# Kernel tuning notes

Hardware: AMD Instinct MI355X
Metric: run time of the kernel (lower is better)

Reference implementation:

```python
import jax, jax.numpy as jnp
import numpy as np

N_SLOTS = 24   # n_slots from __init__
N_ITERS = 25   # fixed Lloyd iterations (stand-in for sklearn max_iter/convergence)
NORM_EPS = 1e-12  # torch F.normalize eps


def setup_inputs() -> dict:
    key = jax.random.key(0)
    features = jax.random.normal(key, (32, 4096, 256), dtype=jnp.float32)
    return {"features": features}


def _pairwise_sqdist(x, x_sq, centers):
    # x: [B,N,D], x_sq: [B,N,1], centers: [B,K,D] -> [B,N,K]
    c_sq = jnp.sum(centers * centers, axis=-1)  # [B,K]
    return x_sq - 2.0 * jnp.einsum('bnd,bkd->bnk', x, centers) + c_sq[:, None, :]


def _kmeans_batched(x, k, n_iters):
    # x: [B,N,D] -> centers [B,K,D], assignments [B,N]
    B, N, D = x.shape
    # deterministic init: K evenly-spaced points per batch item
    init_idx = jnp.linspace(0, N - 1, k).astype(jnp.int32)
    centers0 = x[:, init_idx, :]  # [B,K,D]
    x_sq = jnp.sum(x * x, axis=-1, keepdims=True)  # [B,N,1]

    def step(centers, _):
        d = _pairwise_sqdist(x, x_sq, centers)          # [B,N,K]
        assign = jnp.argmin(d, axis=-1)                 # [B,N]
        onehot = jax.nn.one_hot(assign, k, dtype=x.dtype)  # [B,N,K]
        counts = jnp.sum(onehot, axis=1)                # [B,K]
        sums = jnp.einsum('bnk,bnd->bkd', onehot, x)    # [B,K,D] scatter-mean numerator
        new_centers = sums / jnp.maximum(counts, 1.0)[..., None]
        # empty clusters keep their previous center
        new_centers = jnp.where(counts[..., None] > 0, new_centers, centers)
        return new_centers, None

    centers, _ = jax.lax.scan(step, centers0, None, length=n_iters)
    final_assign = jnp.argmin(_pairwise_sqdist(x, x_sq, centers), axis=-1)
    return centers, final_assign


def reference(features):
    # L2-normalize along feature dim (use_l2_normalization=True)
    norm = jnp.sqrt(jnp.sum(features * features, axis=-1, keepdims=True))
    f = features / jnp.maximum(norm, NORM_EPS)
    # original detaches before clustering (sklearn on CPU): no gradient flow
    f = jax.lax.stop_gradient(f)
    centers, assign = _kmeans_batched(f, N_SLOTS, N_ITERS)
    # slot masks: one_hot then transpose(-2,-1) -> [B, K, N] float32
    slot_masks = jax.nn.one_hot(assign, N_SLOTS, dtype=jnp.float32).transpose(0, 2, 1)
    return centers, slot_masks
```

## Files before the change

### kernel.cpp

```cpp
#include <hip/hip_runtime.h>
#include <math.h>


#define BATCH 32
#define NPTS 4096
#define DIM 256
#define NSLOT 24
#define NITER 25

__global__ __launch_bounds__(256) void k_norm(const float* __restrict__ feat,
                                              double* __restrict__ inv_norm) {
  int lane = threadIdx.x & 63;
  int wid = threadIdx.x >> 6;
  int p = blockIdx.x * 4 + wid;
  const float4 v = *(const float4*)(feat + (size_t)p * DIM + lane * 4);
  double s = (double)v.x * v.x + (double)v.y * v.y + (double)v.z * v.z + (double)v.w * v.w;
#pragma unroll
  for (int m = 32; m; m >>= 1) s += __shfl_xor(s, m);
  if (lane == 0) inv_norm[p] = 1.0 / fmax(sqrt(s), 1e-12);
}

__device__ __forceinline__ double block_sum_256(double v, double* red) {
#pragma unroll
  for (int m = 32; m; m >>= 1) v += __shfl_xor(v, m);
  int w = threadIdx.x >> 6;
  if ((threadIdx.x & 63) == 0) red[w] = v;
  __syncthreads();
  return red[0] + red[1] + red[2] + red[3];
}

__global__ __launch_bounds__(256) void k_init_centers(const float* __restrict__ feat,
                                                      const double* __restrict__ inv_norm,
                                                      double* __restrict__ centers,
                                                      float* __restrict__ cT32,
                                                      float* __restrict__ c_sq32) {
  __shared__ double red[4];
  int t = threadIdx.x, k = blockIdx.x, b = blockIdx.y;
  int idx = (int)((double)k * (NPTS - 1) / (NSLOT - 1));
  double v = (double)feat[((size_t)b * NPTS + idx) * DIM + t] * inv_norm[b * NPTS + idx];
  centers[((size_t)b * NSLOT + k) * DIM + t] = v;
  cT32[((size_t)b * DIM + t) * NSLOT + k] = (float)v;
  double s = block_sum_256(v * v, red);
  if (t == 0) c_sq32[b * NSLOT + k] = (float)s;
}

__global__ __launch_bounds__(256) void k_transpose(const float* __restrict__ feat,
                                                   float* __restrict__ xT) {
  __shared__ float tile[64][65];
  int ix = threadIdx.x & 63, iy = threadIdx.x >> 6;
  int bx = blockIdx.x, by = blockIdx.y, b = blockIdx.z;
  const float* fb = feat + ((size_t)b * NPTS + bx * 64) * DIM + by * 64;
#pragma unroll
  for (int r = 0; r < 64; r += 4)
    tile[r + iy][ix] = fb[(size_t)(r + iy) * DIM + ix];
  __syncthreads();
  float* xb = xT + ((size_t)b * DIM + by * 64) * NPTS + bx * 64;
#pragma unroll
  for (int r = 0; r < 64; r += 4)
    xb[(size_t)(r + iy) * NPTS + ix] = tile[ix][r + iy];
}

template <bool USE_T>
__global__ __launch_bounds__(256) void k_assign(const float* __restrict__ feat,
                                                const float* __restrict__ xT,
                                                const double* __restrict__ inv_norm,
                                                const float* __restrict__ cT32,
                                                const float* __restrict__ c_sq32,
                                                int* __restrict__ assign) {
  __shared__ float part[3][64][NSLOT + 1];
  int lane = threadIdx.x & 63;
  int q = __builtin_amdgcn_readfirstlane(threadIdx.x >> 6);
  int blk = blockIdx.x, b = blockIdx.y;
  int n = blk * 64 + lane;
  const float* cb = cT32 + ((size_t)b * DIM + q * 64) * NSLOT;

  float dot[NSLOT];
#pragma unroll
  for (int k = 0; k < NSLOT; ++k) dot[k] = 0.0f;

  for (int d = 0; d < 64; d += 4) {
    float x0, x1, x2, x3;
    if (USE_T) {
      const float* xp = xT + ((size_t)b * DIM + q * 64 + d) * NPTS + n;
      x0 = xp[0]; x1 = xp[NPTS]; x2 = xp[2 * NPTS]; x3 = xp[3 * NPTS];
    } else {
      float4 v = *(const float4*)(feat + ((size_t)b * NPTS + n) * DIM + q * 64 + d);
      x0 = v.x; x1 = v.y; x2 = v.z; x3 = v.w;
    }
    const float* cp = cb + (size_t)d * NSLOT;
#pragma unroll
    for (int k = 0; k < NSLOT; ++k) {
      float s = dot[k];
      s = fmaf(x0, cp[k], s);
      s = fmaf(x1, cp[NSLOT + k], s);
      s = fmaf(x2, cp[2 * NSLOT + k], s);
      s = fmaf(x3, cp[3 * NSLOT + k], s);
      dot[k] = s;
    }
  }

  if (q) {
#pragma unroll
    for (int k = 0; k < NSLOT; ++k) part[q - 1][lane][k] = dot[k];
  }
  __syncthreads();

  if (q == 0) {
    float inv = (float)inv_norm[b * NPTS + n];
    const float* csq = c_sq32 + b * NSLOT;
    int a = 0;
    float best = 0.0f;
#pragma unroll
    for (int k = 0; k < NSLOT; ++k) {
      float df = dot[k] + part[0][lane][k] + part[1][lane][k] + part[2][lane][k];
      float s = csq[k] - 2.0f * (df * inv);
      if (k == 0) { best = s; }
      else if (s < best) { best = s; a = k; }
    }
    assign[b * NPTS + n] = a;
  }
}

__global__ __launch_bounds__(256) void k_cluster(const float* __restrict__ feat,
                                                 const double* __restrict__ inv_norm,
                                                 const int* __restrict__ assign,
                                                 double* __restrict__ centers,
                                                 float* __restrict__ cT32,
                                                 float* __restrict__ c_sq32) {
  __shared__ int list[NPTS];
  __shared__ int wtot[4];
  __shared__ double part[4][DIM];
  __shared__ double red[4];

  int id = blockIdx.x;
  int xcd = id & 7;
  int r = id >> 3;
  int k = r % NSLOT;
  int b = (r / NSLOT) * 8 + xcd;

  int t = threadIdx.x;
  int lane = t & 63;
  int w = __builtin_amdgcn_readfirstlane(t >> 6);

  const int* ab = assign + b * NPTS;
  int base = 0;
  for (int rr = 0; rr < NPTS / 256; ++rr) {
    int a = ab[rr * 256 + t];
    bool m = (a == k);
    unsigned long long bal = __ballot(m);
    int rank = __popcll(bal & ((1ull << lane) - 1ull));
    if (lane == 0) wtot[w] = __popcll(bal);
    __syncthreads();
    int off = base;
#pragma unroll
    for (int w2 = 0; w2 < 3; ++w2)
      if (w2 < w) off += wtot[w2];
    if (m) list[off + rank] = rr * 256 + t;
    base += wtot[0] + wtot[1] + wtot[2] + wtot[3];
    __syncthreads();
  }
  int mcount = base;

  const float* fb = feat + (size_t)b * NPTS * DIM + lane * 4;
  const double* ib = inv_norm + b * NPTS;
  double a0 = 0.0, a1 = 0.0, a2 = 0.0, a3 = 0.0;

  for (int i = w; i < mcount; i += 8) {
    int n0 = __builtin_amdgcn_readfirstlane(list[i]);
    bool have1 = (i + 4) < mcount;
    int n1 = __builtin_amdgcn_readfirstlane(have1 ? list[i + 4] : list[i]);
    float4 v0 = *(const float4*)(fb + (size_t)n0 * DIM);
    float4 v1 = *(const float4*)(fb + (size_t)n1 * DIM);
    double i0 = ib[n0];
    double i1 = ib[n1];
    a0 += (double)v0.x * i0; a1 += (double)v0.y * i0;
    a2 += (double)v0.z * i0; a3 += (double)v0.w * i0;
    if (have1) {
      a0 += (double)v1.x * i1; a1 += (double)v1.y * i1;
      a2 += (double)v1.z * i1; a3 += (double)v1.w * i1;
    }
  }

  part[w][lane * 4 + 0] = a0;
  part[w][lane * 4 + 1] = a1;
  part[w][lane * 4 + 2] = a2;
  part[w][lane * 4 + 3] = a3;
  __syncthreads();

  double s = ((part[0][t] + part[1][t]) + part[2][t]) + part[3][t];

  size_t ci = ((size_t)b * NSLOT + k) * DIM + t;
  double nc = (mcount > 0) ? (s / (double)mcount) : centers[ci];
  centers[ci] = nc;
  cT32[((size_t)b * DIM + t) * NSLOT + k] = (float)nc;
  double sq = block_sum_256(nc * nc, red);
  if (t == 0) c_sq32[b * NSLOT + k] = (float)sq;
}

__global__ __launch_bounds__(256) void k_mask(const int* __restrict__ assign,
                                              float* __restrict__ masks) {
  int t = threadIdx.x, nc = blockIdx.x, k = blockIdx.y, b = blockIdx.z;
  int n = nc * 256 + t;
  masks[((size_t)b * NSLOT + k) * NPTS + n] = (assign[b * NPTS + n] == k) ? 1.0f : 0.0f;
}

__global__ __launch_bounds__(256) void k_copyc(const double* __restrict__ centers,
                                               float* __restrict__ out_centers) {
  int t = threadIdx.x, k = blockIdx.x, b = blockIdx.y;
  size_t i = ((size_t)b * NSLOT + k) * DIM + t;
  out_centers[i] = (float)centers[i];
}

extern "C" void kernel_launch(void* const* d_in, const int* in_sizes, int n_in,
                              void* d_out, int out_size, void* d_ws, size_t ws_size,
                              hipStream_t stream) {
  (void)in_sizes; (void)n_in; (void)out_size;
  const float* feat = (const float*)d_in[0];
  float* out_centers = (float*)d_out;
  float* out_masks = out_centers + (size_t)BATCH * NSLOT * DIM;

  char* ws = (char*)d_ws;
  double* inv_norm = (double*)ws; ws += (size_t)BATCH * NPTS * 8;
  double* centers  = (double*)ws; ws += (size_t)BATCH * NSLOT * DIM * 8;
  float* cT32      = (float*)ws;  ws += (size_t)BATCH * DIM * NSLOT * 4;
  float* c_sq32    = (float*)ws;  ws += (size_t)BATCH * NSLOT * 4;
  int* assign      = (int*)ws;    ws += (size_t)BATCH * NPTS * 4;
  float* xT        = (float*)ws;
  size_t need_xT = (size_t)(ws - (char*)d_ws) + (size_t)BATCH * DIM * NPTS * 4;
  bool useT = ws_size >= need_xT;

  k_norm<<<BATCH * NPTS / 4, 256, 0, stream>>>(feat, inv_norm);
  k_init_centers<<<dim3(NSLOT, BATCH), 256, 0, stream>>>(feat, inv_norm, centers,
                                                         cT32, c_sq32);
  if (useT)
    k_transpose<<<dim3(NPTS / 64, DIM / 64, BATCH), 256, 0, stream>>>(feat, xT);

  for (int it = 0; it <= NITER; ++it) {
    if (useT)
      k_assign<true><<<dim3(NPTS / 64, BATCH), 256, 0, stream>>>(feat, xT, inv_norm,
                                                                 cT32, c_sq32, assign);
    else
      k_assign<false><<<dim3(NPTS / 64, BATCH), 256, 0, stream>>>(feat, xT, inv_norm,
                                                                  cT32, c_sq32, assign);
    if (it == NITER) break;
    k_cluster<<<NSLOT * BATCH, 256, 0, stream>>>(feat, inv_norm, assign,
                                                 centers, cT32, c_sq32);
  }

  k_mask<<<dim3(NPTS / 256, NSLOT, BATCH), 256, 0, stream>>>(assign, out_masks);
  k_copyc<<<dim3(NSLOT, BATCH), 256, 0, stream>>>(centers, out_centers);
}
```

Baseline: 1.862 ms.

## Split cluster accumulation into point quarters with separate reduction kernel

The per-cluster center update is split so each (batch, slot) is handled by four blocks, each scanning a quarter of the points, writing partial sums and counts to global memory. A new small kernel combines the four partials and computes the new centers, the transposed fp32 copy and the squared norms. The gather loop is unrolled to four rows per step and the assign kernel's inner loop now loads 8 dims per iteration. This raises the block count for the gather phase and its memory-level parallelism, at the cost of an extra launch per iteration and a partial-sum buffer round trip. The XCD-aware batch mapping is dropped.

```diff
diff --git a/kernel.cpp b/kernel.cpp
--- a/kernel.cpp
+++ b/kernel.cpp
@@ -7,6 +7,7 @@
 #define DIM 256
 #define NSLOT 24
 #define NITER 25
+#define QPTS 1024
 
 __global__ __launch_bounds__(256) void k_norm(const float* __restrict__ feat,
                                               double* __restrict__ inv_norm) {
@@ -78,23 +79,24 @@
 #pragma unroll
   for (int k = 0; k < NSLOT; ++k) dot[k] = 0.0f;
 
-  for (int d = 0; d < 64; d += 4) {
-    float x0, x1, x2, x3;
+  for (int d = 0; d < 64; d += 8) {
+    float x[8];
     if (USE_T) {
       const float* xp = xT + ((size_t)b * DIM + q * 64 + d) * NPTS + n;
-      x0 = xp[0]; x1 = xp[NPTS]; x2 = xp[2 * NPTS]; x3 = xp[3 * NPTS];
+#pragma unroll
+      for (int j = 0; j < 8; ++j) x[j] = xp[(size_t)j * NPTS];
     } else {
       float4 v = *(const float4*)(feat + ((size_t)b * NPTS + n) * DIM + q * 64 + d);
-      x0 = v.x; x1 = v.y; x2 = v.z; x3 = v.w;
+      float4 u = *(const float4*)(feat + ((size_t)b * NPTS + n) * DIM + q * 64 + d + 4);
+      x[0] = v.x; x[1] = v.y; x[2] = v.z; x[3] = v.w;
+      x[4] = u.x; x[5] = u.y; x[6] = u.z; x[7] = u.w;
     }
     const float* cp = cb + (size_t)d * NSLOT;
 #pragma unroll
     for (int k = 0; k < NSLOT; ++k) {
       float s = dot[k];
-      s = fmaf(x0, cp[k], s);
-      s = fmaf(x1, cp[NSLOT + k], s);
-      s = fmaf(x2, cp[2 * NSLOT + k], s);
-      s = fmaf(x3, cp[3 * NSLOT + k], s);
+#pragma unroll
+      for (int j = 0; j < 8; ++j) s = fmaf(x[j], cp[j * NSLOT + k], s);
       dot[k] = s;
     }
   }
@@ -121,32 +123,29 @@
   }
 }
 
-__global__ __launch_bounds__(256) void k_cluster(const float* __restrict__ feat,
-                                                 const double* __restrict__ inv_norm,
-                                                 const int* __restrict__ assign,
-                                                 double* __restrict__ centers,
-                                                 float* __restrict__ cT32,
-                                                 float* __restrict__ c_sq32) {
-  __shared__ int list[NPTS];
+__global__ __launch_bounds__(256) void k_cluster4(const float* __restrict__ feat,
+                                                  const double* __restrict__ inv_norm,
+                                                  const int* __restrict__ assign,
+                                                  double* __restrict__ psumG,
+                                                  int* __restrict__ cntG) {
+  __shared__ unsigned short list[QPTS];
   __shared__ int wtot[4];
   __shared__ double part[4][DIM];
-  __shared__ double red[4];
 
   int id = blockIdx.x;
-  int xcd = id & 7;
-  int r = id >> 3;
+  int q = id & 3;
+  int r = id >> 2;
   int k = r % NSLOT;
-  int b = (r / NSLOT) * 8 + xcd;
+  int b = r / NSLOT;
 
   int t = threadIdx.x;
   int lane = t & 63;
   int w = __builtin_amdgcn_readfirstlane(t >> 6);
 
-  const int* ab = assign + b * NPTS;
+  const int* ab = assign + b * NPTS + q * QPTS;
   int base = 0;
-  for (int rr = 0; rr < NPTS / 256; ++rr) {
-    int a = ab[rr * 256 + t];
-    bool m = (a == k);
+  for (int rr = 0; rr < QPTS / 256; ++rr) {
+    bool m = (ab[rr * 256 + t] == k);
     unsigned long long bal = __ballot(m);
     int rank = __popcll(bal & ((1ull << lane) - 1ull));
     if (lane == 0) wtot[w] = __popcll(bal);
@@ -155,30 +154,35 @@
 #pragma unroll
     for (int w2 = 0; w2 < 3; ++w2)
       if (w2 < w) off += wtot[w2];
-    if (m) list[off + rank] = rr * 256 + t;
+    if (m) list[off + rank] = (unsigned short)(rr * 256 + t);
     base += wtot[0] + wtot[1] + wtot[2] + wtot[3];
     __syncthreads();
   }
   int mcount = base;
 
-  const float* fb = feat + (size_t)b * NPTS * DIM + lane * 4;
-  const double* ib = inv_norm + b * NPTS;
+  const float* fb = feat + ((size_t)b * NPTS + q * QPTS) * DIM + lane * 4;
+  const double* ib = inv_norm + b * NPTS + q * QPTS;
   double a0 = 0.0, a1 = 0.0, a2 = 0.0, a3 = 0.0;
 
-  for (int i = w; i < mcount; i += 8) {
-    int n0 = __builtin_amdgcn_readfirstlane(list[i]);
-    bool have1 = (i + 4) < mcount;
-    int n1 = __builtin_amdgcn_readfirstlane(have1 ? list[i + 4] : list[i]);
+  for (int i = w; i < mcount; i += 16) {
+    bool h1 = (i + 4) < mcount, h2 = (i + 8) < mcount, h3 = (i + 12) < mcount;
+    int n0 = __builtin_amdgcn_readfirstlane((int)list[i]);
+    int n1 = __builtin_amdgcn_readfirstlane((int)list[h1 ? i + 4 : i]);
+    int n2 = __builtin_amdgcn_readfirstlane((int)list[h2 ? i + 8 : i]);
+    int n3 = __builtin_amdgcn_readfirstlane((int)list[h3 ? i + 12 : i]);
     float4 v0 = *(const float4*)(fb + (size_t)n0 * DIM);
     float4 v1 = *(const float4*)(fb + (size_t)n1 * DIM);
-    double i0 = ib[n0];
-    double i1 = ib[n1];
+    float4 v2 = *(const float4*)(fb + (size_t)n2 * DIM);
+    float4 v3 = *(const float4*)(fb + (size_t)n3 * DIM);
+    double i0 = ib[n0], i1 = ib[n1], i2 = ib[n2], i3 = ib[n3];
     a0 += (double)v0.x * i0; a1 += (double)v0.y * i0;
     a2 += (double)v0.z * i0; a3 += (double)v0.w * i0;
-    if (have1) {
-      a0 += (double)v1.x * i1; a1 += (double)v1.y * i1;
-      a2 += (double)v1.z * i1; a3 += (double)v1.w * i1;
-    }
+    if (h1) { a0 += (double)v1.x * i1; a1 += (double)v1.y * i1;
+              a2 += (double)v1.z * i1; a3 += (double)v1.w * i1; }
+    if (h2) { a0 += (double)v2.x * i2; a1 += (double)v2.y * i2;
+              a2 += (double)v2.z * i2; a3 += (double)v2.w * i2; }
+    if (h3) { a0 += (double)v3.x * i3; a1 += (double)v3.y * i3;
+              a2 += (double)v3.z * i3; a3 += (double)v3.w * i3; }
   }
 
   part[w][lane * 4 + 0] = a0;
@@ -188,9 +192,24 @@
   __syncthreads();
 
   double s = ((part[0][t] + part[1][t]) + part[2][t]) + part[3][t];
+  psumG[(size_t)id * DIM + t] = s;
+  if (t == 0) cntG[id] = mcount;
+}
+
+__global__ __launch_bounds__(256) void k_upd2(const double* __restrict__ psumG,
+                                              const int* __restrict__ cntG,
+                                              double* __restrict__ centers,
+                                              float* __restrict__ cT32,
+                                              float* __restrict__ c_sq32) {
+  __shared__ double red[4];
+  int t = threadIdx.x, k = blockIdx.x, b = blockIdx.y;
+  int id = (b * NSLOT + k) * 4;
+  const double* p = psumG + (size_t)id * DIM;
+  double s = ((p[t] + p[DIM + t]) + p[2 * DIM + t]) + p[3 * DIM + t];
+  int cnt = cntG[id] + cntG[id + 1] + cntG[id + 2] + cntG[id + 3];
 
   size_t ci = ((size_t)b * NSLOT + k) * DIM + t;
-  double nc = (mcount > 0) ? (s / (double)mcount) : centers[ci];
+  double nc = (cnt > 0) ? (s / (double)cnt) : centers[ci];
   centers[ci] = nc;
   cT32[((size_t)b * DIM + t) * NSLOT + k] = (float)nc;
   double sq = block_sum_256(nc * nc, red);
@@ -225,6 +244,8 @@
   float* cT32      = (float*)ws;  ws += (size_t)BATCH * DIM * NSLOT * 4;
   float* c_sq32    = (float*)ws;  ws += (size_t)BATCH * NSLOT * 4;
   int* assign      = (int*)ws;    ws += (size_t)BATCH * NPTS * 4;
+  double* psumG    = (double*)ws; ws += (size_t)BATCH * NSLOT * 4 * DIM * 8;
+  int* cntG        = (int*)ws;    ws += (size_t)BATCH * NSLOT * 4 * 4;
   float* xT        = (float*)ws;
   size_t need_xT = (size_t)(ws - (char*)d_ws) + (size_t)BATCH * DIM * NPTS * 4;
   bool useT = ws_size >= need_xT;
@@ -243,8 +264,9 @@
       k_assign<false><<<dim3(NPTS / 64, BATCH), 256, 0, stream>>>(feat, xT, inv_norm,
                                                                   cT32, c_sq32, assign);
     if (it == NITER) break;
-    k_cluster<<<NSLOT * BATCH, 256, 0, stream>>>(feat, inv_norm, assign,
-                                                 centers, cT32, c_sq32);
+    k_cluster4<<<NSLOT * BATCH * 4, 256, 0, stream>>>(feat, inv_norm, assign,
+                                                      psumG, cntG);
+    k_upd2<<<dim3(NSLOT, BATCH), 256, 0, stream>>>(psumG, cntG, centers, cT32, c_sq32);
   }
 
   k_mask<<<dim3(NPTS / 256, NSLOT, BATCH), 256, 0, stream>>>(assign, out_masks);
```

Measured after the change: 1.730 ms. -7.1%, faster.
